# Optimization experiments

Hardware: AMD Instinct MI355X
Metric: run time of the kernel (lower is better)

Reference implementation:

```python
import jax, jax.numpy as jnp
import numpy as np

J = 25
C_IN, HID, LAT = 3, 64, 32


def _graph_conv(x, A, W, b):
    # x: [N,T,J,Cin]; A: [J,J]; W: [Cin,Cout]; b: [Cout]
    A = jax.nn.softmax(A, axis=-1)
    # fused adjacency mix + projection: (A @ x) @ W + b
    x = jnp.einsum('ij,ntjc->ntic', A, x)
    return jnp.einsum('ntjc,cd->ntjd', x, W) + b


def setup_inputs() -> dict:
    key = jax.random.key(0)
    ks = jax.random.split(key, 13)
    x = jax.random.normal(ks[0], (32, 2048, J, C_IN), dtype=jnp.float32)
    eye = jnp.eye(J, dtype=jnp.float32)
    def lin(kw, kb, cin, cout):
        W = jax.random.normal(kw, (cin, cout), dtype=jnp.float32) / np.sqrt(cin)
        b = jax.random.normal(kb, (cout,), dtype=jnp.float32) * 0.01
        return W, b
    W1, b1 = lin(ks[1], ks[2], C_IN, HID)
    W2, b2 = lin(ks[3], ks[4], HID, LAT)
    W3, b3 = lin(ks[5], ks[6], LAT, HID)
    W4, b4 = lin(ks[7], ks[8], HID, C_IN)
    return {
        'x': x,
        'A1': eye, 'W1': W1, 'b1': b1,
        'A2': eye, 'W2': W2, 'b2': b2,
        'A3': eye, 'W3': W3, 'b3': b3,
        'A4': eye, 'W4': W4, 'b4': b4,
    }


def reference(x, A1, W1, b1, A2, W2, b2, A3, W3, b3, A4, W4, b4):
    h = jax.nn.relu(_graph_conv(x, A1, W1, b1))     # encoder_g1 + relu
    z = _graph_conv(h, A2, W2, b2)                  # encoder_g2 (no relu)
    h_dec = jax.nn.relu(_graph_conv(z, A3, W3, b3)) # decoder_g1 + relu
    out = _graph_conv(h_dec, A4, W4, b4)            # decoder_g2
    return out
```

## Files before the change

### kernel.cpp

```cpp
#include <hip/hip_runtime.h>
#include <math.h>

#define J 25
#define NJC 75
#define NWAVE 4
#define NTHREADS 256
#define NFPW 8
#define SCRW 2112

#define O_A1T  0
#define O_APP  1024
#define O_A4B  2048
#define O_W2T  3072
#define O_W3T  5120
#define O_W1T  7168
#define O_W4C  8192
#define O_BPPB 8448
#define O_B4   8512

using bf16x4 = __attribute__((ext_vector_type(4))) __bf16;
using bf16x8 = __attribute__((ext_vector_type(8))) __bf16;
using f32x16 = __attribute__((ext_vector_type(16))) float;

__device__ inline bf16x8 zero8() {
    bf16x8 z;
    #pragma unroll
    for (int j = 0; j < 8; j++) z[j] = (__bf16)0.f;
    return z;
}

__global__ void gcn_precompute(
    const float* __restrict__ A1, const float* __restrict__ W1, const float* __restrict__ b1,
    const float* __restrict__ A2, const float* __restrict__ W2, const float* __restrict__ b2,
    const float* __restrict__ A3, const float* __restrict__ W3, const float* __restrict__ b3,
    const float* __restrict__ A4, const float* __restrict__ W4, const float* __restrict__ b4,
    __bf16* __restrict__ cw)
{
    __shared__ float T[3125];
    __shared__ float bpp[64];
    float* T0 = T;        float* T1 = T + 625;  float* T2 = T + 1250;
    float* T3 = T + 1875; float* T4 = T + 2500;
    const int t = threadIdx.x;

    if (t < 100) {
        const int m = t / J, i = t % J;
        const float* Asrc = (m == 0) ? A1 : (m == 1) ? A2 : (m == 2) ? A3 : A4;
        float row[J];
        float mx = -1e30f;
        #pragma unroll
        for (int j = 0; j < J; j++) { row[j] = Asrc[i * J + j]; mx = fmaxf(mx, row[j]); }
        float s = 0.f;
        #pragma unroll
        for (int j = 0; j < J; j++) { row[j] = __expf(row[j] - mx); s += row[j]; }
        const float inv = 1.f / s;
        float* dst = T + m * 625 + i * J;
        #pragma unroll
        for (int j = 0; j < J; j++) dst[j] = row[j] * inv;
    }
    if (t < 64) {
        float s = b3[t];
        #pragma unroll
        for (int l = 0; l < 32; l++) s += W3[l * 64 + t] * b2[l];
        bpp[t] = s;
    }
    __syncthreads();

    for (int idx = t; idx < 625; idx += 256) {
        const int i = idx / J, jj = idx % J;
        float s = 0.f;
        #pragma unroll
        for (int k = 0; k < J; k++) s += T2[i * J + k] * T1[k * J + jj];
        T4[idx] = s;
    }
    __syncthreads();

    for (int i = t; i < 1024; i += 256) {
        const int b = i >> 8, n = (i >> 3) & 31, jj = i & 7, j = 8 * b + jj;
        const bool ok = (j < J) && (n < J);
        cw[O_A1T + i] = (__bf16)(ok ? T0[n * J + j] : 0.f);
        cw[O_APP + i] = (__bf16)(ok ? T4[n * J + j] : 0.f);
        cw[O_A4B + i] = (__bf16)(ok ? T3[n * J + j] : 0.f);
    }
    for (int i = t; i < 2048; i += 256) {
        const int b = i >> 8, m = (i >> 3) & 31, jj = i & 7;
        cw[O_W2T + i] = (__bf16)W2[(8 * b + jj) * 32 + m];
        const int tt = i >> 10, r = i & 1023;
        const int b3i = r >> 8, m3 = (r >> 3) & 31, j3 = r & 7;
        cw[O_W3T + i] = (__bf16)W3[(8 * b3i + j3) * 64 + tt * 32 + m3];
    }
    for (int i = t; i < 1024; i += 256) {
        const int tt = i >> 9, r = i & 511, hf = r >> 8, q = r & 255;
        const int m = q >> 3, c = q & 7, d = tt * 32 + m;
        float v = 0.f;
        if (hf == 0) {
            if (c < 3) v = W1[c * 64 + d];
            else if (c == 3) v = b1[d];
        }
        cw[O_W1T + i] = (__bf16)v;
    }
    if (t < 256)
        cw[O_W4C + t] = (t < 192) ? (__bf16)W4[(t & 63) * 3 + (t >> 6)] : (__bf16)0.f;

    if (t < 64) {
        const int tt = t >> 5, rem = t & 31, hf = rem >> 4, q = rem & 15;
        const int g = q >> 2, r2 = q & 3;
        cw[O_BPPB + t] = (__bf16)bpp[tt * 32 + 8 * g + 4 * hf + r2];
    }
    float* fb4 = (float*)(cw + O_B4);
    if (t >= 64 && t < 68) fb4[t - 64] = (t < 67) ? b4[t - 64] : 0.f;
}

__global__ __launch_bounds__(NTHREADS, 3) void gcn_fused(
    const float* __restrict__ x,
    const __bf16* __restrict__ cw,
    float* __restrict__ out)
{
    __shared__ __align__(16) __bf16 SCR[NWAVE * SCRW];

    const int t = threadIdx.x;
    const int w = t >> 6, lane = t & 63, ln = lane & 31, half = lane >> 5;
    const int fo = ln * 8;
    __bf16* sc = &SCR[w * SCRW];

    const long fbase = ((long)blockIdx.x * NWAVE + w) * NFPW;

    long xb = fbase * NJC;
    float xv0 = x[xb + lane];
    float xv1 = (lane < NJC - 64) ? x[xb + 64 + lane] : 0.f;

    bf16x8 rA1T[2], rApp[2], rA4b[2], rW1[2], rW2[4], rW3[4], rW4[4], rBpp[4];
    #pragma unroll
    for (int ks = 0; ks < 2; ks++) {
        rA1T[ks] = *(const bf16x8*)&cw[O_A1T + (2 * ks + half) * 256 + fo];
        rApp[ks] = *(const bf16x8*)&cw[O_APP + (2 * ks + half) * 256 + fo];
        rA4b[ks] = *(const bf16x8*)&cw[O_A4B + (2 * ks + half) * 256 + fo];
        rW1[ks]  = *(const bf16x8*)&cw[O_W1T + ks * 512 + half * 256 + fo];
    }
    #pragma unroll
    for (int ks = 0; ks < 4; ks++)
        rW2[ks] = *(const bf16x8*)&cw[O_W2T + (half + 2 * ks) * 256 + fo];
    #pragma unroll
    for (int tt = 0; tt < 2; tt++)
        #pragma unroll
        for (int ks = 0; ks < 2; ks++)
            rW3[tt * 2 + ks] = *(const bf16x8*)&cw[O_W3T + tt * 1024 + (half + 2 * ks) * 256 + fo];
    #pragma unroll
    for (int ks = 0; ks < 4; ks++) {
        rW4[ks] = zero8();
        if (ln < 3) rW4[ks] = *(const bf16x8*)&cw[O_W4C + ln * 64 + (half + 2 * ks) * 8];
    }
    #pragma unroll
    for (int tt = 0; tt < 2; tt++)
        #pragma unroll
        for (int p = 0; p < 2; p++)
            rBpp[tt * 2 + p] = *(const bf16x8*)&cw[O_BPPB + (tt * 2 + half) * 16 + p * 8];
    float b4v = 0.f;
    if (ln < 3) b4v = ((const float*)(cw + O_B4))[ln];

    f32x16 Z;
    #pragma unroll
    for (int z = 0; z < 16; z++) Z[z] = 0.f;

    for (int fi = 0; fi < NFPW; fi++) {
        const long f = fbase + fi;

        {
            const int i0 = lane, c0 = i0 % 3, j0 = i0 / 3;
            sc[(j0 >> 3) * 264 + c0 * 8 + (j0 & 7)] = (__bf16)xv0;
            if (lane < NJC - 64) {
                const int i1 = 64 + lane, c1 = i1 % 3, j1 = i1 / 3;
                sc[(j1 >> 3) * 264 + c1 * 8 + (j1 & 7)] = (__bf16)xv1;
            }
            if (half == 0) sc[(ln >> 3) * 264 + 24 + (ln & 7)] = (ln < J) ? (__bf16)1.f : (__bf16)0.f;
            if (lane < 21) sc[3 * 264 + (lane / 7) * 8 + 1 + (lane % 7)] = (__bf16)0.f;
        }

        float nxv0 = 0.f, nxv1 = 0.f;
        if (fi + 1 < NFPW) {
            const long nxb = (f + 1) * NJC;
            nxv0 = x[nxb + lane];
            if (lane < NJC - 64) nxv1 = x[nxb + 64 + lane];
        }

        f32x16 accY;
        {
            bf16x8 a0 = *(const bf16x8*)&sc[half * 264 + fo];
            accY = __builtin_amdgcn_mfma_f32_32x32x16_bf16(a0, rA1T[0], Z, 0, 0, 0);
            bf16x8 a1 = *(const bf16x8*)&sc[(2 + half) * 264 + fo];
            accY = __builtin_amdgcn_mfma_f32_32x32x16_bf16(a1, rA1T[1], accY, 0, 0, 0);
        }

        bf16x8 yb;
        #pragma unroll
        for (int jj = 0; jj < 8; jj++)
            yb[jj] = (half == 0 && jj < 4) ? (__bf16)accY[jj] : (__bf16)0.f;
        #pragma unroll
        for (int tt = 0; tt < 2; tt++) {
            f32x16 acc = __builtin_amdgcn_mfma_f32_32x32x16_bf16(rW1[tt], yb, Z, 0, 0, 0);
            #pragma unroll
            for (int g = 0; g < 4; g++) {
                bf16x4 p;
                #pragma unroll
                for (int r2 = 0; r2 < 4; r2++) p[r2] = (__bf16)fmaxf(acc[4 * g + r2], 0.f);
                *(bf16x4*)&sc[(tt * 4 + g) * 264 + fo + 4 * half] = p;
            }
        }

        f32x16 accU;
        {
            bf16x8 a0 = *(const bf16x8*)&sc[half * 264 + fo];
            accU = __builtin_amdgcn_mfma_f32_32x32x16_bf16(a0, rW2[0], Z, 0, 0, 0);
            #pragma unroll
            for (int ks = 1; ks < 4; ks++) {
                bf16x8 a = *(const bf16x8*)&sc[(half + 2 * ks) * 264 + fo];
                accU = __builtin_amdgcn_mfma_f32_32x32x16_bf16(a, rW2[ks], accU, 0, 0, 0);
            }
        }
        #pragma unroll
        for (int g = 0; g < 4; g++) {
            bf16x4 p;
            #pragma unroll
            for (int r2 = 0; r2 < 4; r2++) p[r2] = (__bf16)accU[4 * g + r2];
            *(bf16x4*)&sc[g * 264 + fo + 4 * half] = p;
        }

        f32x16 accV;
        {
            bf16x8 a0 = *(const bf16x8*)&sc[half * 264 + fo];
            accV = __builtin_amdgcn_mfma_f32_32x32x16_bf16(a0, rApp[0], Z, 0, 0, 0);
            bf16x8 a1 = *(const bf16x8*)&sc[(2 + half) * 264 + fo];
            accV = __builtin_amdgcn_mfma_f32_32x32x16_bf16(a1, rApp[1], accV, 0, 0, 0);
        }
        #pragma unroll
        for (int g = 0; g < 4; g++) {
            bf16x4 p;
            #pragma unroll
            for (int r2 = 0; r2 < 4; r2++) p[r2] = (__bf16)accV[4 * g + r2];
            *(bf16x4*)&sc[(4 + g) * 264 + fo + 4 * half] = p;
        }

        bf16x8 vb0 = *(const bf16x8*)&sc[(4 + half) * 264 + fo];
        bf16x8 vb1 = *(const bf16x8*)&sc[(6 + half) * 264 + fo];
        #pragma unroll
        for (int tt = 0; tt < 2; tt++) {
            f32x16 acc = __builtin_amdgcn_mfma_f32_32x32x16_bf16(rW3[tt * 2 + 0], vb0, Z, 0, 0, 0);
            acc = __builtin_amdgcn_mfma_f32_32x32x16_bf16(rW3[tt * 2 + 1], vb1, acc, 0, 0, 0);
            #pragma unroll
            for (int g = 0; g < 4; g++) {
                bf16x4 p;
                #pragma unroll
                for (int r2 = 0; r2 < 4; r2++) {
                    const int q = g * 4 + r2;
                    const float bias = (float)rBpp[tt * 2 + (q >> 3)][q & 7];
                    p[r2] = (__bf16)fmaxf(acc[4 * g + r2] + bias, 0.f);
                }
                *(bf16x4*)&sc[(tt * 4 + g) * 264 + fo + 4 * half] = p;
            }
        }

        f32x16 accP;
        {
            bf16x8 a0 = *(const bf16x8*)&sc[half * 264 + fo];
            accP = __builtin_amdgcn_mfma_f32_32x32x16_bf16(a0, rW4[0], Z, 0, 0, 0);
            #pragma unroll
            for (int ks = 1; ks < 4; ks++) {
                bf16x8 a = *(const bf16x8*)&sc[(half + 2 * ks) * 264 + fo];
                accP = __builtin_amdgcn_mfma_f32_32x32x16_bf16(a, rW4[ks], accP, 0, 0, 0);
            }
        }
        #pragma unroll
        for (int g = 0; g < 4; g++) {
            bf16x4 p;
            #pragma unroll
            for (int r2 = 0; r2 < 4; r2++) p[r2] = (__bf16)accP[4 * g + r2];
            *(bf16x4*)&sc[g * 264 + fo + 4 * half] = p;
        }

        f32x16 accO;
        {
            bf16x8 b0 = *(const bf16x8*)&sc[half * 264 + fo];
            accO = __builtin_amdgcn_mfma_f32_32x32x16_bf16(rA4b[0], b0, Z, 0, 0, 0);
            bf16x8 b1 = *(const bf16x8*)&sc[(2 + half) * 264 + fo];
            accO = __builtin_amdgcn_mfma_f32_32x32x16_bf16(rA4b[1], b1, accO, 0, 0, 0);
        }
        if (ln < 3) {
            const long ob = f * NJC;
            #pragma unroll
            for (int r = 0; r < 16; r++) {
                const int row = (r & 3) + 8 * (r >> 2) + 4 * half;
                if (row < J) out[ob + row * 3 + ln] = accO[r] + b4v;
            }
        }

        xv0 = nxv0; xv1 = nxv1;
    }
}

extern "C" void kernel_launch(void* const* d_in, const int* in_sizes, int n_in,
                              void* d_out, int out_size, void* d_ws, size_t ws_size,
                              hipStream_t stream)
{
    const float* x  = (const float*)d_in[0];
    const float* A1 = (const float*)d_in[1];
    const float* W1 = (const float*)d_in[2];
    const float* b1 = (const float*)d_in[3];
    const float* A2 = (const float*)d_in[4];
    const float* W2 = (const float*)d_in[5];
    const float* b2 = (const float*)d_in[6];
    const float* A3 = (const float*)d_in[7];
    const float* W3 = (const float*)d_in[8];
    const float* b3 = (const float*)d_in[9];
    const float* A4 = (const float*)d_in[10];
    const float* W4 = (const float*)d_in[11];
    const float* b4 = (const float*)d_in[12];
    float* out = (float*)d_out;
    __bf16* cw = (__bf16*)d_ws;

    const int NT = in_sizes[0] / NJC;
    const int nblocks = NT / (NWAVE * NFPW);

    gcn_precompute<<<1, 256, 0, stream>>>(
        A1, W1, b1, A2, W2, b2, A3, W3, b3, A4, W4, b4, cw);
    gcn_fused<<<nblocks, NTHREADS, 0, stream>>>(x, cw, out);
}
```

Baseline: 153.7 us.

## Pass MFMA intermediates between layers via cross-lane shuffles instead of LDS

Replaces the LDS scratch round-trips between chained MFMA stages with an in-register swap: accumulators are packed to bf16 pairs and exchanged between the two half-waves with __shfl, producing the operand fragments for the next MFMA directly. This removes most LDS writes and reads per frame and halves the per-wave scratch size. The cost is extra shuffle and select instructions plus higher register pressure, and the fragment mapping must match exactly for the result to stay correct.

Measured after the change: 165.5 us. 1.08x slower.

```diff
diff --git a/kernel.cpp b/kernel.cpp
--- a/kernel.cpp
+++ b/kernel.cpp
@@ -6,7 +6,7 @@
 #define NWAVE 4
 #define NTHREADS 256
 #define NFPW 8
-#define SCRW 2112
+#define SCRW 1056
 
 #define O_A1T  0
 #define O_APP  1024
@@ -27,6 +27,32 @@
     #pragma unroll
     for (int j = 0; j < 8; j++) z[j] = (__bf16)0.f;
     return z;
+}
+
+__device__ inline unsigned pkbf(float a, float b) {
+    union { __bf16 h; unsigned short u; } ua, ub;
+    ua.h = (__bf16)a; ub.h = (__bf16)b;
+    return (unsigned)ua.u | ((unsigned)ub.u << 16);
+}
+
+__device__ inline void cswap(const f32x16 acc, int half, int lx,
+                             bf16x8* f0, bf16x8* f1) {
+    const unsigned p0 = pkbf(acc[0],  acc[1]),  p1 = pkbf(acc[2],  acc[3]);
+    const unsigned p2 = pkbf(acc[4],  acc[5]),  p3 = pkbf(acc[6],  acc[7]);
+    const unsigned p4 = pkbf(acc[8],  acc[9]),  p5 = pkbf(acc[10], acc[11]);
+    const unsigned p6 = pkbf(acc[12], acc[13]), p7 = pkbf(acc[14], acc[15]);
+    const unsigned s0 = half ? p0 : p2, s1 = half ? p1 : p3;
+    const unsigned s2 = half ? p4 : p6, s3 = half ? p5 : p7;
+    const unsigned r0 = (unsigned)__shfl((int)s0, lx, 64);
+    const unsigned r1 = (unsigned)__shfl((int)s1, lx, 64);
+    const unsigned r2 = (unsigned)__shfl((int)s2, lx, 64);
+    const unsigned r3 = (unsigned)__shfl((int)s3, lx, 64);
+    uint4 u0, u1;
+    u0.x = half ? r0 : p0;  u0.y = half ? r1 : p1;
+    u0.z = half ? p2 : r0;  u0.w = half ? p3 : r1;
+    u1.x = half ? r2 : p4;  u1.y = half ? r3 : p5;
+    u1.z = half ? p6 : r2;  u1.w = half ? p7 : r3;
+    *f0 = *(bf16x8*)&u0;  *f1 = *(bf16x8*)&u1;
 }
 
 __global__ void gcn_precompute(
@@ -119,6 +145,7 @@
 
     const int t = threadIdx.x;
     const int w = t >> 6, lane = t & 63, ln = lane & 31, half = lane >> 5;
+    const int lx = lane ^ 32;
     const int fo = ln * 8;
     __bf16* sc = &SCR[w * SCRW];
 
@@ -194,95 +221,49 @@
         #pragma unroll
         for (int jj = 0; jj < 8; jj++)
             yb[jj] = (half == 0 && jj < 4) ? (__bf16)accY[jj] : (__bf16)0.f;
+        bf16x8 hf[4];
         #pragma unroll
         for (int tt = 0; tt < 2; tt++) {
             f32x16 acc = __builtin_amdgcn_mfma_f32_32x32x16_bf16(rW1[tt], yb, Z, 0, 0, 0);
             #pragma unroll
-            for (int g = 0; g < 4; g++) {
-                bf16x4 p;
-                #pragma unroll
-                for (int r2 = 0; r2 < 4; r2++) p[r2] = (__bf16)fmaxf(acc[4 * g + r2], 0.f);
-                *(bf16x4*)&sc[(tt * 4 + g) * 264 + fo + 4 * half] = p;
+            for (int z = 0; z < 16; z++) acc[z] = fmaxf(acc[z], 0.f);
+            cswap(acc, half, lx, &hf[tt * 2], &hf[tt * 2 + 1]);
+        }
+
+        f32x16 accU = __builtin_amdgcn_mfma_f32_32x32x16_bf16(hf[0], rW2[0], Z, 0, 0, 0);
+        #pragma unroll
+        for (int ks = 1; ks < 4; ks++)
+            accU = __builtin_amdgcn_mfma_f32_32x32x16_bf16(hf[ks], rW2[ks], accU, 0, 0, 0);
+        bf16x8 uf[2];
+        cswap(accU, half, lx, &uf[0], &uf[1]);
+
+        f32x16 accV = __builtin_amdgcn_mfma_f32_32x32x16_bf16(uf[0], rApp[0], Z, 0, 0, 0);
+        accV = __builtin_amdgcn_mfma_f32_32x32x16_bf16(uf[1], rApp[1], accV, 0, 0, 0);
+        bf16x8 vf[2];
+        cswap(accV, half, lx, &vf[0], &vf[1]);
+
+        bf16x8 hd[4];
+        #pragma unroll
+        for (int tt = 0; tt < 2; tt++) {
+            f32x16 acc = __builtin_amdgcn_mfma_f32_32x32x16_bf16(rW3[tt * 2 + 0], vf[0], Z, 0, 0, 0);
+            acc = __builtin_amdgcn_mfma_f32_32x32x16_bf16(rW3[tt * 2 + 1], vf[1], acc, 0, 0, 0);
+            #pragma unroll
+            for (int q = 0; q < 16; q++) {
+                const float bias = (float)rBpp[tt * 2 + (q >> 3)][q & 7];
+                acc[q] = fmaxf(acc[q] + bias, 0.f);
             }
-        }
-
-        f32x16 accU;
-        {
-            bf16x8 a0 = *(const bf16x8*)&sc[half * 264 + fo];
-            accU = __builtin_amdgcn_mfma_f32_32x32x16_bf16(a0, rW2[0], Z, 0, 0, 0);
-            #pragma unroll
-            for (int ks = 1; ks < 4; ks++) {
-                bf16x8 a = *(const bf16x8*)&sc[(half + 2 * ks) * 264 + fo];
-                accU = __builtin_amdgcn_mfma_f32_32x32x16_bf16(a, rW2[ks], accU, 0, 0, 0);
-            }
-        }
-        #pragma unroll
-        for (int g = 0; g < 4; g++) {
-            bf16x4 p;
-            #pragma unroll
-            for (int r2 = 0; r2 < 4; r2++) p[r2] = (__bf16)accU[4 * g + r2];
-            *(bf16x4*)&sc[g * 264 + fo + 4 * half] = p;
-        }
-
-        f32x16 accV;
-        {
-            bf16x8 a0 = *(const bf16x8*)&sc[half * 264 + fo];
-            accV = __builtin_amdgcn_mfma_f32_32x32x16_bf16(a0, rApp[0], Z, 0, 0, 0);
-            bf16x8 a1 = *(const bf16x8*)&sc[(2 + half) * 264 + fo];
-            accV = __builtin_amdgcn_mfma_f32_32x32x16_bf16(a1, rApp[1], accV, 0, 0, 0);
-        }
-        #pragma unroll
-        for (int g = 0; g < 4; g++) {
-            bf16x4 p;
-            #pragma unroll
-            for (int r2 = 0; r2 < 4; r2++) p[r2] = (__bf16)accV[4 * g + r2];
-            *(bf16x4*)&sc[(4 + g) * 264 + fo + 4 * half] = p;
-        }
-
-        bf16x8 vb0 = *(const bf16x8*)&sc[(4 + half) * 264 + fo];
-        bf16x8 vb1 = *(const bf16x8*)&sc[(6 + half) * 264 + fo];
-        #pragma unroll
-        for (int tt = 0; tt < 2; tt++) {
-            f32x16 acc = __builtin_amdgcn_mfma_f32_32x32x16_bf16(rW3[tt * 2 + 0], vb0, Z, 0, 0, 0);
-            acc = __builtin_amdgcn_mfma_f32_32x32x16_bf16(rW3[tt * 2 + 1], vb1, acc, 0, 0, 0);
-            #pragma unroll
-            for (int g = 0; g < 4; g++) {
-                bf16x4 p;
-                #pragma unroll
-                for (int r2 = 0; r2 < 4; r2++) {
-                    const int q = g * 4 + r2;
-                    const float bias = (float)rBpp[tt * 2 + (q >> 3)][q & 7];
-                    p[r2] = (__bf16)fmaxf(acc[4 * g + r2] + bias, 0.f);
-                }
-                *(bf16x4*)&sc[(tt * 4 + g) * 264 + fo + 4 * half] = p;
-            }
-        }
-
-        f32x16 accP;
-        {
-            bf16x8 a0 = *(const bf16x8*)&sc[half * 264 + fo];
-            accP = __builtin_amdgcn_mfma_f32_32x32x16_bf16(a0, rW4[0], Z, 0, 0, 0);
-            #pragma unroll
-            for (int ks = 1; ks < 4; ks++) {
-                bf16x8 a = *(const bf16x8*)&sc[(half + 2 * ks) * 264 + fo];
-                accP = __builtin_amdgcn_mfma_f32_32x32x16_bf16(a, rW4[ks], accP, 0, 0, 0);
-            }
-        }
-        #pragma unroll
-        for (int g = 0; g < 4; g++) {
-            bf16x4 p;
-            #pragma unroll
-            for (int r2 = 0; r2 < 4; r2++) p[r2] = (__bf16)accP[4 * g + r2];
-            *(bf16x4*)&sc[g * 264 + fo + 4 * half] = p;
-        }
-
-        f32x16 accO;
-        {
-            bf16x8 b0 = *(const bf16x8*)&sc[half * 264 + fo];
-            accO = __builtin_amdgcn_mfma_f32_32x32x16_bf16(rA4b[0], b0, Z, 0, 0, 0);
-            bf16x8 b1 = *(const bf16x8*)&sc[(2 + half) * 264 + fo];
-            accO = __builtin_amdgcn_mfma_f32_32x32x16_bf16(rA4b[1], b1, accO, 0, 0, 0);
-        }
+            cswap(acc, half, lx, &hd[tt * 2], &hd[tt * 2 + 1]);
+        }
+
+        f32x16 accP = __builtin_amdgcn_mfma_f32_32x32x16_bf16(hd[0], rW4[0], Z, 0, 0, 0);
+        #pragma unroll
+        for (int ks = 1; ks < 4; ks++)
+            accP = __builtin_amdgcn_mfma_f32_32x32x16_bf16(hd[ks], rW4[ks], accP, 0, 0, 0);
+        bf16x8 pf[2];
+        cswap(accP, half, lx, &pf[0], &pf[1]);
+
+        f32x16 accO = __builtin_amdgcn_mfma_f32_32x32x16_bf16(rA4b[0], pf[0], Z, 0, 0, 0);
+        accO = __builtin_amdgcn_mfma_f32_32x32x16_bf16(rA4b[1], pf[1], accO, 0, 0, 0);
         if (ln < 3) {
             const long ob = f * NJC;
             #pragma unroll
```

## Interleave two frames per wave iteration to hide MFMA dependency latency

Applied to the files above, without the earlier changes.

Each wave now processes two frames per loop iteration, using two separate LDS scratch regions and interleaving their MFMA chains so independent matrix ops can issue back to back. The next pair of input frames is prefetched, and loop-invariant scatter offsets are hoisted out of the loop. The aim is to cover the serial dependency latency of the per-frame MFMA chain. In exchange, register and LDS use per wave roughly double and the occupancy hint drops from 3 to 2 blocks. The per-frame zeroing of the padded scratch entries is also dropped.

After: 155.7 us. No clear change (+1.3%).

```diff
diff --git a/kernel.cpp b/kernel.cpp
--- a/kernel.cpp
+++ b/kernel.cpp
@@ -6,7 +6,7 @@
 #define NWAVE 4
 #define NTHREADS 256
 #define NFPW 8
-#define SCRW 2112
+#define SCRW 4224
 
 #define O_A1T  0
 #define O_APP  1024
@@ -110,7 +110,7 @@
     if (t >= 64 && t < 68) fb4[t - 64] = (t < 67) ? b4[t - 64] : 0.f;
 }
 
-__global__ __launch_bounds__(NTHREADS, 3) void gcn_fused(
+__global__ __launch_bounds__(NTHREADS, 2) void gcn_fused(
     const float* __restrict__ x,
     const __bf16* __restrict__ cw,
     float* __restrict__ out)
@@ -120,13 +120,16 @@
     const int t = threadIdx.x;
     const int w = t >> 6, lane = t & 63, ln = lane & 31, half = lane >> 5;
     const int fo = ln * 8;
-    __bf16* sc = &SCR[w * SCRW];
+    __bf16* sa = &SCR[w * SCRW];
+    __bf16* sb = sa + 8 * 264;
 
     const long fbase = ((long)blockIdx.x * NWAVE + w) * NFPW;
 
     long xb = fbase * NJC;
-    float xv0 = x[xb + lane];
-    float xv1 = (lane < NJC - 64) ? x[xb + 64 + lane] : 0.f;
+    float xa0 = x[xb + lane];
+    float xa1 = (lane < NJC - 64) ? x[xb + 64 + lane] : 0.f;
+    float xb0 = x[xb + NJC + lane];
+    float xb1 = (lane < NJC - 64) ? x[xb + NJC + 64 + lane] : 0.f;
 
     bf16x8 rA1T[2], rApp[2], rA4b[2], rW1[2], rW2[4], rW3[4], rW4[4], rBpp[4];
     #pragma unroll
@@ -161,138 +164,191 @@
     #pragma unroll
     for (int z = 0; z < 16; z++) Z[z] = 0.f;
 
-    for (int fi = 0; fi < NFPW; fi++) {
-        const long f = fbase + fi;
-
-        {
-            const int i0 = lane, c0 = i0 % 3, j0 = i0 / 3;
-            sc[(j0 >> 3) * 264 + c0 * 8 + (j0 & 7)] = (__bf16)xv0;
+    const int c0 = lane % 3, j0 = lane / 3;
+    const int sc0 = (j0 >> 3) * 264 + c0 * 8 + (j0 & 7);
+    const int i1 = 64 + lane, c1 = i1 % 3, j1 = i1 / 3;
+    const int sc1 = (j1 >> 3) * 264 + c1 * 8 + (j1 & 7);
+    const int so = (ln >> 3) * 264 + 24 + (ln & 7);
+    const __bf16 ov = (ln < J) ? (__bf16)1.f : (__bf16)0.f;
+
+    for (int fi = 0; fi < NFPW; fi += 2) {
+        const long fA = fbase + fi, fB = fA + 1;
+
+        sa[sc0] = (__bf16)xa0;
+        sb[sc0] = (__bf16)xb0;
+        if (lane < NJC - 64) { sa[sc1] = (__bf16)xa1; sb[sc1] = (__bf16)xb1; }
+        if (half == 0) { sa[so] = ov; sb[so] = ov; }
+
+        float nxa0 = 0.f, nxa1 = 0.f, nxb0 = 0.f, nxb1 = 0.f;
+        if (fi + 2 < NFPW) {
+            const long nxb_ = (fA + 2) * NJC;
+            nxa0 = x[nxb_ + lane];
+            nxb0 = x[nxb_ + NJC + lane];
             if (lane < NJC - 64) {
-                const int i1 = 64 + lane, c1 = i1 % 3, j1 = i1 / 3;
-                sc[(j1 >> 3) * 264 + c1 * 8 + (j1 & 7)] = (__bf16)xv1;
-            }
-            if (half == 0) sc[(ln >> 3) * 264 + 24 + (ln & 7)] = (ln < J) ? (__bf16)1.f : (__bf16)0.f;
-            if (lane < 21) sc[3 * 264 + (lane / 7) * 8 + 1 + (lane % 7)] = (__bf16)0.f;
-        }
-
-        float nxv0 = 0.f, nxv1 = 0.f;
-        if (fi + 1 < NFPW) {
-            const long nxb = (f + 1) * NJC;
-            nxv0 = x[nxb + lane];
-            if (lane < NJC - 64) nxv1 = x[nxb + 64 + lane];
-        }
-
-        f32x16 accY;
-        {
-            bf16x8 a0 = *(const bf16x8*)&sc[half * 264 + fo];
-            accY = __builtin_amdgcn_mfma_f32_32x32x16_bf16(a0, rA1T[0], Z, 0, 0, 0);
-            bf16x8 a1 = *(const bf16x8*)&sc[(2 + half) * 264 + fo];
-            accY = __builtin_amdgcn_mfma_f32_32x32x16_bf16(a1, rA1T[1], accY, 0, 0, 0);
-        }
-
-        bf16x8 yb;
-        #pragma unroll
-        for (int jj = 0; jj < 8; jj++)
-            yb[jj] = (half == 0 && jj < 4) ? (__bf16)accY[jj] : (__bf16)0.f;
+                nxa1 = x[nxb_ + 64 + lane];
+                nxb1 = x[nxb_ + NJC + 64 + lane];
+            }
+        }
+
+        f32x16 accYa, accYb;
+        {
+            bf16x8 a0 = *(const bf16x8*)&sa[half * 264 + fo];
+            bf16x8 b0 = *(const bf16x8*)&sb[half * 264 + fo];
+            accYa = __builtin_amdgcn_mfma_f32_32x32x16_bf16(a0, rA1T[0], Z, 0, 0, 0);
+            accYb = __builtin_amdgcn_mfma_f32_32x32x16_bf16(b0, rA1T[0], Z, 0, 0, 0);
+            bf16x8 a1 = *(const bf16x8*)&sa[(2 + half) * 264 + fo];
+            bf16x8 b1 = *(const bf16x8*)&sb[(2 + half) * 264 + fo];
+            accYa = __builtin_amdgcn_mfma_f32_32x32x16_bf16(a1, rA1T[1], accYa, 0, 0, 0);
+            accYb = __builtin_amdgcn_mfma_f32_32x32x16_bf16(b1, rA1T[1], accYb, 0, 0, 0);
+        }
+
+        bf16x8 yba, ybb;
+        #pragma unroll
+        for (int jj = 0; jj < 8; jj++) {
+            yba[jj] = (half == 0 && jj < 4) ? (__bf16)accYa[jj] : (__bf16)0.f;
+            ybb[jj] = (half == 0 && jj < 4) ? (__bf16)accYb[jj] : (__bf16)0.f;
+        }
         #pragma unroll
         for (int tt = 0; tt < 2; tt++) {
-            f32x16 acc = __builtin_amdgcn_mfma_f32_32x32x16_bf16(rW1[tt], yb, Z, 0, 0, 0);
+            f32x16 acca = __builtin_amdgcn_mfma_f32_32x32x16_bf16(rW1[tt], yba, Z, 0, 0, 0);
+            f32x16 accb = __builtin_amdgcn_mfma_f32_32x32x16_bf16(rW1[tt], ybb, Z, 0, 0, 0);
             #pragma unroll
             for (int g = 0; g < 4; g++) {
-                bf16x4 p;
+                bf16x4 pa, pb;
                 #pragma unroll
-                for (int r2 = 0; r2 < 4; r2++) p[r2] = (__bf16)fmaxf(acc[4 * g + r2], 0.f);
-                *(bf16x4*)&sc[(tt * 4 + g) * 264 + fo + 4 * half] = p;
-            }
-        }
-
-        f32x16 accU;
-        {
-            bf16x8 a0 = *(const bf16x8*)&sc[half * 264 + fo];
-            accU = __builtin_amdgcn_mfma_f32_32x32x16_bf16(a0, rW2[0], Z, 0, 0, 0);
+                for (int r2 = 0; r2 < 4; r2++) {
+                    pa[r2] = (__bf16)fmaxf(acca[4 * g + r2], 0.f);
+                    pb[r2] = (__bf16)fmaxf(accb[4 * g + r2], 0.f);
+                }
+                *(bf16x4*)&sa[(tt * 4 + g) * 264 + fo + 4 * half] = pa;
+                *(bf16x4*)&sb[(tt * 4 + g) * 264 + fo + 4 * half] = pb;
+            }
+        }
+
+        f32x16 accUa, accUb;
+        {
+            bf16x8 a0 = *(const bf16x8*)&sa[half * 264 + fo];
+            bf16x8 b0 = *(const bf16x8*)&sb[half * 264 + fo];
+            accUa = __builtin_amdgcn_mfma_f32_32x32x16_bf16(a0, rW2[0], Z, 0, 0, 0);
+            accUb = __builtin_amdgcn_mfma_f32_32x32x16_bf16(b0, rW2[0], Z, 0, 0, 0);
             #pragma unroll
             for (int ks = 1; ks < 4; ks++) {
-                bf16x8 a = *(const bf16x8*)&sc[(half + 2 * ks) * 264 + fo];
-                accU = __builtin_amdgcn_mfma_f32_32x32x16_bf16(a, rW2[ks], accU, 0, 0, 0);
+                bf16x8 a = *(const bf16x8*)&sa[(half + 2 * ks) * 264 + fo];
+                bf16x8 b = *(const bf16x8*)&sb[(half + 2 * ks) * 264 + fo];
+                accUa = __builtin_amdgcn_mfma_f32_32x32x16_bf16(a, rW2[ks], accUa, 0, 0, 0);
+                accUb = __builtin_amdgcn_mfma_f32_32x32x16_bf16(b, rW2[ks], accUb, 0, 0, 0);
             }
         }
         #pragma unroll
         for (int g = 0; g < 4; g++) {
-            bf16x4 p;
-            #pragma unroll
-            for (int r2 = 0; r2 < 4; r2++) p[r2] = (__bf16)accU[4 * g + r2];
-            *(bf16x4*)&sc[g * 264 + fo + 4 * half] = p;
-        }
-
-        f32x16 accV;
-        {
-            bf16x8 a0 = *(const bf16x8*)&sc[half * 264 + fo];
-            accV = __builtin_amdgcn_mfma_f32_32x32x16_bf16(a0, rApp[0], Z, 0, 0, 0);
-            bf16x8 a1 = *(const bf16x8*)&sc[(2 + half) * 264 + fo];
-            accV = __builtin_amdgcn_mfma_f32_32x32x16_bf16(a1, rApp[1], accV, 0, 0, 0);
+            bf16x4 pa, pb;
+            #pragma unroll
+            for (int r2 = 0; r2 < 4; r2++) {
+                pa[r2] = (__bf16)accUa[4 * g + r2];
+                pb[r2] = (__bf16)accUb[4 * g + r2];
+            }
+            *(bf16x4*)&sa[g * 264 + fo + 4 * half] = pa;
+            *(bf16x4*)&sb[g * 264 + fo + 4 * half] = pb;
+        }
+
+        f32x16 accVa, accVb;
+        {
+            bf16x8 a0 = *(const bf16x8*)&sa[half * 264 + fo];
+            bf16x8 b0 = *(const bf16x8*)&sb[half * 264 + fo];
+            accVa = __builtin_amdgcn_mfma_f32_32x32x16_bf16(a0, rApp[0], Z, 0, 0, 0);
+            accVb = __builtin_amdgcn_mfma_f32_32x32x16_bf16(b0, rApp[0], Z, 0, 0, 0);
+            bf16x8 a1 = *(const bf16x8*)&sa[(2 + half) * 264 + fo];
+            bf16x8 b1 = *(const bf16x8*)&sb[(2 + half) * 264 + fo];
+            accVa = __builtin_amdgcn_mfma_f32_32x32x16_bf16(a1, rApp[1], accVa, 0, 0, 0);
+            accVb = __builtin_amdgcn_mfma_f32_32x32x16_bf16(b1, rApp[1], accVb, 0, 0, 0);
         }
         #pragma unroll
         for (int g = 0; g < 4; g++) {
-            bf16x4 p;
-            #pragma unroll
-            for (int r2 = 0; r2 < 4; r2++) p[r2] = (__bf16)accV[4 * g + r2];
-            *(bf16x4*)&sc[(4 + g) * 264 + fo + 4 * half] = p;
-        }
-
-        bf16x8 vb0 = *(const bf16x8*)&sc[(4 + half) * 264 + fo];
-        bf16x8 vb1 = *(const bf16x8*)&sc[(6 + half) * 264 + fo];
+            bf16x4 pa, pb;
+            #pragma unroll
+            for (int r2 = 0; r2 < 4; r2++) {
+                pa[r2] = (__bf16)accVa[4 * g + r2];
+                pb[r2] = (__bf16)accVb[4 * g + r2];
+            }
+            *(bf16x4*)&sa[(4 + g) * 264 + fo + 4 * half] = pa;
+            *(bf16x4*)&sb[(4 + g) * 264 + fo + 4 * half] = pb;
+        }
+
+        bf16x8 va0 = *(const bf16x8*)&sa[(4 + half) * 264 + fo];
+        bf16x8 va1 = *(const bf16x8*)&sa[(6 + half) * 264 + fo];
+        bf16x8 vb0 = *(const bf16x8*)&sb[(4 + half) * 264 + fo];
+        bf16x8 vb1 = *(const bf16x8*)&sb[(6 + half) * 264 + fo];
         #pragma unroll
         for (int tt = 0; tt < 2; tt++) {
-            f32x16 acc = __builtin_amdgcn_mfma_f32_32x32x16_bf16(rW3[tt * 2 + 0], vb0, Z, 0, 0, 0);
-            acc = __builtin_amdgcn_mfma_f32_32x32x16_bf16(rW3[tt * 2 + 1], vb1, acc, 0, 0, 0);
+            f32x16 acca = __builtin_amdgcn_mfma_f32_32x32x16_bf16(rW3[tt * 2 + 0], va0, Z, 0, 0, 0);
+            f32x16 accb = __builtin_amdgcn_mfma_f32_32x32x16_bf16(rW3[tt * 2 + 0], vb0, Z, 0, 0, 0);
+            acca = __builtin_amdgcn_mfma_f32_32x32x16_bf16(rW3[tt * 2 + 1], va1, acca, 0, 0, 0);
+            accb = __builtin_amdgcn_mfma_f32_32x32x16_bf16(rW3[tt * 2 + 1], vb1, accb, 0, 0, 0);
             #pragma unroll
             for (int g = 0; g < 4; g++) {
-                bf16x4 p;
+                bf16x4 pa, pb;
                 #pragma unroll
                 for (int r2 = 0; r2 < 4; r2++) {
                     const int q = g * 4 + r2;
                     const float bias = (float)rBpp[tt * 2 + (q >> 3)][q & 7];
-                    p[r2] = (__bf16)fmaxf(acc[4 * g + r2] + bias, 0.f);
+                    pa[r2] = (__bf16)fmaxf(acca[4 * g + r2] + bias, 0.f);
+                    pb[r2] = (__bf16)fmaxf(accb[4 * g + r2] + bias, 0.f);
                 }
-                *(bf16x4*)&sc[(tt * 4 + g) * 264 + fo + 4 * half] = p;
-            }
-        }
-
-        f32x16 accP;
-        {
-            bf16x8 a0 = *(const bf16x8*)&sc[half * 264 + fo];
-            accP = __builtin_amdgcn_mfma_f32_32x32x16_bf16(a0, rW4[0], Z, 0, 0, 0);
+                *(bf16x4*)&sa[(tt * 4 + g) * 264 + fo + 4 * half] = pa;
+                *(bf16x4*)&sb[(tt * 4 + g) * 264 + fo + 4 * half] = pb;
+            }
+        }
+
+        f32x16 accPa, accPb;
+        {
+            bf16x8 a0 = *(const bf16x8*)&sa[half * 264 + fo];
+            bf16x8 b0 = *(const bf16x8*)&sb[half * 264 + fo];
+            accPa = __builtin_amdgcn_mfma_f32_32x32x16_bf16(a0, rW4[0], Z, 0, 0, 0);
+            accPb = __builtin_amdgcn_mfma_f32_32x32x16_bf16(b0, rW4[0], Z, 0, 0, 0);
             #pragma unroll
             for (int ks = 1; ks < 4; ks++) {
-                bf16x8 a = *(const bf16x8*)&sc[(half + 2 * ks) * 264 + fo];
-                accP = __builtin_amdgcn_mfma_f32_32x32x16_bf16(a, rW4[ks], accP, 0, 0, 0);
+                bf16x8 a = *(const bf16x8*)&sa[(half + 2 * ks) * 264 + fo];
+                bf16x8 b = *(const bf16x8*)&sb[(half + 2 * ks) * 264 + fo];
+                accPa = __builtin_amdgcn_mfma_f32_32x32x16_bf16(a, rW4[ks], accPa, 0, 0, 0);
+                accPb = __builtin_amdgcn_mfma_f32_32x32x16_bf16(b, rW4[ks], accPb, 0, 0, 0);
             }
         }
         #pragma unroll
         for (int g = 0; g < 4; g++) {
-            bf16x4 p;
-            #pragma unroll
-            for (int r2 = 0; r2 < 4; r2++) p[r2] = (__bf16)accP[4 * g + r2];
-            *(bf16x4*)&sc[g * 264 + fo + 4 * half] = p;
-        }
-
-        f32x16 accO;
-        {
-            bf16x8 b0 = *(const bf16x8*)&sc[half * 264 + fo];
-            accO = __builtin_amdgcn_mfma_f32_32x32x16_bf16(rA4b[0], b0, Z, 0, 0, 0);
-            bf16x8 b1 = *(const bf16x8*)&sc[(2 + half) * 264 + fo];
-            accO = __builtin_amdgcn_mfma_f32_32x32x16_bf16(rA4b[1], b1, accO, 0, 0, 0);
+            bf16x4 pa, pb;
+            #pragma unroll
+            for (int r2 = 0; r2 < 4; r2++) {
+                pa[r2] = (__bf16)accPa[4 * g + r2];
+                pb[r2] = (__bf16)accPb[4 * g + r2];
+            }
+            *(bf16x4*)&sa[g * 264 + fo + 4 * half] = pa;
+            *(bf16x4*)&sb[g * 264 + fo + 4 * half] = pb;
+        }
+
+        f32x16 accOa, accOb;
+        {
+            bf16x8 a0 = *(const bf16x8*)&sa[half * 264 + fo];
+            bf16x8 b0 = *(const bf16x8*)&sb[half * 264 + fo];
+            accOa = __builtin_amdgcn_mfma_f32_32x32x16_bf16(rA4b[0], a0, Z, 0, 0, 0);
+            accOb = __builtin_amdgcn_mfma_f32_32x32x16_bf16(rA4b[0], b0, Z, 0, 0, 0);
+            bf16x8 a1 = *(const bf16x8*)&sa[(2 + half) * 264 + fo];
+            bf16x8 b1 = *(const bf16x8*)&sb[(2 + half) * 264 + fo];
+            accOa = __builtin_amdgcn_mfma_f32_32x32x16_bf16(rA4b[1], a1, accOa, 0, 0, 0);
+            accOb = __builtin_amdgcn_mfma_f32_32x32x16_bf16(rA4b[1], b1, accOb, 0, 0, 0);
         }
         if (ln < 3) {
-            const long ob = f * NJC;
+            const long oa = fA * NJC, ob = fB * NJC;
             #pragma unroll
             for (int r = 0; r < 16; r++) {
                 const int row = (r & 3) + 8 * (r >> 2) + 4 * half;
-                if (row < J) out[ob + row * 3 + ln] = accO[r] + b4v;
-            }
-        }
-
-        xv0 = nxv0; xv1 = nxv1;
+                if (row < J) {
+                    out[oa + row * 3 + ln] = accOa[r] + b4v;
+                    out[ob + row * 3 + ln] = accOb[r] + b4v;
+                }
+            }
+        }
+
+        xa0 = nxa0; xa1 = nxa1; xb0 = nxb0; xb1 = nxb1;
     }
 }
 
```

## Pre-transpose input into bf16 MFMA operand layout via separate prep kernel

Applied to the files above, without the earlier changes.

Adds a kernel that converts x into a padded bf16 layout matching the first MFMA's operand format, including the ones row used for the bias. The fused kernel can then load operands straight into registers and skip the LDS scatter/gather for the first layer. It also halves frames per wave and raises the occupancy hint to 4 blocks per CU. In exchange it adds an extra kernel launch and a full read of x plus a write and re-read of a bf16 copy through the workspace, and it falls back to the old path if the workspace is too small.

Result: slower. 217.4 us (+41.5%).

```diff
diff --git a/kernel.cpp b/kernel.cpp
--- a/kernel.cpp
+++ b/kernel.cpp
@@ -5,7 +5,7 @@
 #define NJC 75
 #define NWAVE 4
 #define NTHREADS 256
-#define NFPW 8
+#define NFPW 4
 #define SCRW 2112
 
 #define O_A1T  0
@@ -17,6 +17,7 @@
 #define O_W4C  8192
 #define O_BPPB 8448
 #define O_B4   8512
+#define XF_OFF 32768
 
 using bf16x4 = __attribute__((ext_vector_type(4))) __bf16;
 using bf16x8 = __attribute__((ext_vector_type(8))) __bf16;
@@ -110,9 +111,28 @@
     if (t >= 64 && t < 68) fb4[t - 64] = (t < 67) ? b4[t - 64] : 0.f;
 }
 
-__global__ __launch_bounds__(NTHREADS, 3) void gcn_fused(
+__global__ void gcn_xprep(const float* __restrict__ x,
+                          __bf16* __restrict__ xf, const int total8)
+{
+    int idx = blockIdx.x * blockDim.x + threadIdx.x;
+    if (idx >= total8) return;
+    const int f = idx >> 4, r = idx & 15;
+    const int m = r >> 2, b = r & 3;
+    bf16x8 v;
+    #pragma unroll
+    for (int jj = 0; jj < 8; jj++) {
+        const int k = 8 * b + jj;
+        float val = 0.f;
+        if (k < J) val = (m < 3) ? x[(long)f * NJC + k * 3 + m] : 1.f;
+        v[jj] = (__bf16)val;
+    }
+    *(bf16x8*)&xf[(long)idx * 8] = v;
+}
+
+__global__ __launch_bounds__(NTHREADS, 4) void gcn_fused(
     const float* __restrict__ x,
     const __bf16* __restrict__ cw,
+    const __bf16* __restrict__ xf,
     float* __restrict__ out)
 {
     __shared__ __align__(16) __bf16 SCR[NWAVE * SCRW];
@@ -124,9 +144,17 @@
 
     const long fbase = ((long)blockIdx.x * NWAVE + w) * NFPW;
 
-    long xb = fbase * NJC;
-    float xv0 = x[xb + lane];
-    float xv1 = (lane < NJC - 64) ? x[xb + 64 + lane] : 0.f;
+    bf16x8 xr0, xr1;
+    float xv0 = 0.f, xv1 = 0.f;
+    if (xf) {
+        const __bf16* xp = xf + fbase * 128 + (ln & 3) * 32;
+        xr0 = *(const bf16x8*)(xp + 8 * half);
+        xr1 = *(const bf16x8*)(xp + 16 + 8 * half);
+    } else {
+        const long xb = fbase * NJC;
+        xv0 = x[xb + lane];
+        xv1 = (lane < NJC - 64) ? x[xb + 64 + lane] : 0.f;
+    }
 
     bf16x8 rA1T[2], rApp[2], rA4b[2], rW1[2], rW2[4], rW3[4], rW4[4], rBpp[4];
     #pragma unroll
@@ -161,34 +189,41 @@
     #pragma unroll
     for (int z = 0; z < 16; z++) Z[z] = 0.f;
 
+    const int c0 = lane % 3, j0 = lane / 3;
+    const int sc0 = (j0 >> 3) * 264 + c0 * 8 + (j0 & 7);
+    const int i1 = 64 + lane, c1 = i1 % 3, j1 = i1 / 3;
+    const int sc1 = (j1 >> 3) * 264 + c1 * 8 + (j1 & 7);
+    const int so = (ln >> 3) * 264 + 24 + (ln & 7);
+    const __bf16 ov = (ln < J) ? (__bf16)1.f : (__bf16)0.f;
+
     for (int fi = 0; fi < NFPW; fi++) {
         const long f = fbase + fi;
 
-        {
-            const int i0 = lane, c0 = i0 % 3, j0 = i0 / 3;
-            sc[(j0 >> 3) * 264 + c0 * 8 + (j0 & 7)] = (__bf16)xv0;
-            if (lane < NJC - 64) {
-                const int i1 = 64 + lane, c1 = i1 % 3, j1 = i1 / 3;
-                sc[(j1 >> 3) * 264 + c1 * 8 + (j1 & 7)] = (__bf16)xv1;
-            }
-            if (half == 0) sc[(ln >> 3) * 264 + 24 + (ln & 7)] = (ln < J) ? (__bf16)1.f : (__bf16)0.f;
-            if (lane < 21) sc[3 * 264 + (lane / 7) * 8 + 1 + (lane % 7)] = (__bf16)0.f;
-        }
-
+        bf16x8 a1op0, a1op1;
+        bf16x8 nxr0, nxr1;
         float nxv0 = 0.f, nxv1 = 0.f;
-        if (fi + 1 < NFPW) {
-            const long nxb = (f + 1) * NJC;
-            nxv0 = x[nxb + lane];
-            if (lane < NJC - 64) nxv1 = x[nxb + 64 + lane];
-        }
-
-        f32x16 accY;
-        {
-            bf16x8 a0 = *(const bf16x8*)&sc[half * 264 + fo];
-            accY = __builtin_amdgcn_mfma_f32_32x32x16_bf16(a0, rA1T[0], Z, 0, 0, 0);
-            bf16x8 a1 = *(const bf16x8*)&sc[(2 + half) * 264 + fo];
-            accY = __builtin_amdgcn_mfma_f32_32x32x16_bf16(a1, rA1T[1], accY, 0, 0, 0);
-        }
+        if (xf) {
+            a1op0 = xr0; a1op1 = xr1;
+            if (fi + 1 < NFPW) {
+                const __bf16* xp = xf + (f + 1) * 128 + (ln & 3) * 32;
+                nxr0 = *(const bf16x8*)(xp + 8 * half);
+                nxr1 = *(const bf16x8*)(xp + 16 + 8 * half);
+            }
+        } else {
+            sc[sc0] = (__bf16)xv0;
+            if (lane < NJC - 64) sc[sc1] = (__bf16)xv1;
+            if (half == 0) sc[so] = ov;
+            if (fi + 1 < NFPW) {
+                const long nxb = (f + 1) * NJC;
+                nxv0 = x[nxb + lane];
+                if (lane < NJC - 64) nxv1 = x[nxb + 64 + lane];
+            }
+            a1op0 = *(const bf16x8*)&sc[half * 264 + fo];
+            a1op1 = *(const bf16x8*)&sc[(2 + half) * 264 + fo];
+        }
+
+        f32x16 accY = __builtin_amdgcn_mfma_f32_32x32x16_bf16(a1op0, rA1T[0], Z, 0, 0, 0);
+        accY = __builtin_amdgcn_mfma_f32_32x32x16_bf16(a1op1, rA1T[1], accY, 0, 0, 0);
 
         bf16x8 yb;
         #pragma unroll
@@ -292,7 +327,7 @@
             }
         }
 
-        xv0 = nxv0; xv1 = nxv1;
+        xr0 = nxr0; xr1 = nxr1; xv0 = nxv0; xv1 = nxv1;
     }
 }
 
@@ -319,7 +354,14 @@
     const int NT = in_sizes[0] / NJC;
     const int nblocks = NT / (NWAVE * NFPW);
 
+    const size_t need = (size_t)XF_OFF + (size_t)NT * 256;
+    __bf16* xfp = (ws_size >= need) ? (__bf16*)((char*)d_ws + XF_OFF) : nullptr;
+
     gcn_precompute<<<1, 256, 0, stream>>>(
         A1, W1, b1, A2, W2, b2, A3, W3, b3, A4, W4, b4, cw);
-    gcn_fused<<<nblocks, NTHREADS, 0, stream>>>(x, cw, out);
-}
+    if (xfp) {
+        const int total8 = NT * 16;
+        gcn_xprep<<<(total8 + 255) / 256, 256, 0, stream>>>(x, xfp, total8);
+    }
+    gcn_fused<<<nblocks, NTHREADS, 0, stream>>>(x, cw, xfp, out);
+}
```
